# Performance work log

Measured on AMD Instinct MI355X. Metric: run time of the kernel, lower is better.

The kernel has to match this reference:

```python
import jax, jax.numpy as jnp
import numpy as np

B, S, D = 4, 2048, 1024
H = 16
HD = D // H  # 64

def setup_inputs() -> dict:
    key = jax.random.key(0)
    ks = jax.random.split(key, 7)
    s = 0.02
    return {
        "x": jax.random.normal(ks[0], (B, S, D), dtype=jnp.float32),
        "Wq": jax.random.normal(ks[1], (D, D), dtype=jnp.float32) * s,
        "bq": jax.random.normal(ks[2], (D,), dtype=jnp.float32) * s,
        "Wk": jax.random.normal(ks[3], (D, D), dtype=jnp.float32) * s,
        "bk": jax.random.normal(ks[4], (D,), dtype=jnp.float32) * s,
        "Wv": jax.random.normal(ks[5], (D, D), dtype=jnp.float32) * s,
        "bv": jax.random.normal(ks[6], (D,), dtype=jnp.float32) * s,
    }

def reference(x, Wq, bq, Wk, bk, Wv, bv):
    bs, seq, _ = x.shape
    q = (x @ Wq.T + bq).reshape(bs, seq, H, HD).transpose(0, 2, 1, 3)  # [b,h,s,d]
    k = (x @ Wk.T + bk).reshape(bs, seq, H, HD).transpose(0, 2, 1, 3)
    v = (x @ Wv.T + bv).reshape(bs, seq, H, HD).transpose(0, 2, 1, 3)
    scores = jnp.einsum('bhqd,bhkd->bhqk', q, k) / jnp.sqrt(jnp.float32(HD))
    probs = jax.nn.softmax(scores, axis=-1)  # dropout p=0 -> identity
    att = jnp.einsum('bhqk,bhkd->bhqd', probs, v)
    return att.transpose(0, 2, 1, 3).reshape(bs, seq, H * HD)
```

## Files before the change

### kernel.cpp

```cpp
#include <hip/hip_runtime.h>

typedef __bf16 bf16x8 __attribute__((ext_vector_type(8)));
typedef float f32x4 __attribute__((ext_vector_type(4)));
typedef float f32x16 __attribute__((ext_vector_type(16)));

#define BATCH 4
#define SEQ   2048
#define DIM   1024
#define NH    16
#define HD    64
#define ECF   0.18033688f

__device__ __forceinline__ unsigned short f2bf(float f) {
  union { float f; unsigned u; } v; v.f = f;
  unsigned u = v.u;
  u += 0x7FFF + ((u >> 16) & 1);
  return (unsigned short)(u >> 16);
}

__device__ __forceinline__ void g2lds16(const unsigned short* g, unsigned short* l) {
  __builtin_amdgcn_global_load_lds(
      (const __attribute__((address_space(1))) unsigned int*)g,
      (__attribute__((address_space(3))) unsigned int*)l, 16, 0, 0);
}

__device__ __forceinline__ unsigned packbf(float a, float b) {
  __bf16 lo = (__bf16)a, hi = (__bf16)b;
  unsigned short ul = __builtin_bit_cast(unsigned short, lo);
  unsigned short uh = __builtin_bit_cast(unsigned short, hi);
  return (unsigned)ul | ((unsigned)uh << 16);
}

__global__ __launch_bounds__(256) void cast_all_kernel(
    const float* __restrict__ x,  const float* __restrict__ Wq,
    const float* __restrict__ Wk, const float* __restrict__ Wv,
    unsigned short* __restrict__ xb,  unsigned short* __restrict__ wqb,
    unsigned short* __restrict__ wkb, unsigned short* __restrict__ wvb) {
  const int XG = (BATCH * SEQ * DIM) / 8;
  const int WG = (DIM * DIM) / 8;
  int i = blockIdx.x * 256 + threadIdx.x;
  const float* in; unsigned short* out; float sc = 1.0f; int off;
  if (i < XG)               { in = x;  out = xb;  off = i; }
  else if (i < XG + WG)     { in = Wq; out = wqb; off = i - XG; sc = ECF; }
  else if (i < XG + 2 * WG) { in = Wk; out = wkb; off = i - XG - WG; }
  else                      { in = Wv; out = wvb; off = i - XG - 2 * WG; }
  const float4* p = (const float4*)in + (size_t)off * 2;
  float4 a = p[0], b = p[1];
  unsigned short r[8];
  r[0] = f2bf(a.x * sc); r[1] = f2bf(a.y * sc); r[2] = f2bf(a.z * sc); r[3] = f2bf(a.w * sc);
  r[4] = f2bf(b.x * sc); r[5] = f2bf(b.y * sc); r[6] = f2bf(b.z * sc); r[7] = f2bf(b.w * sc);
  *(uint4*)&out[(size_t)off * 8] = *(uint4*)r;
}

__global__ __launch_bounds__(256) void gemm_qkv(
    const unsigned short* __restrict__ A,
    const unsigned short* __restrict__ Wqp, const unsigned short* __restrict__ Wkp,
    const unsigned short* __restrict__ Wvp,
    const float* __restrict__ bqp, const float* __restrict__ bkp,
    const float* __restrict__ bvp,
    unsigned short* __restrict__ oq, unsigned short* __restrict__ ok,
    unsigned short* __restrict__ ov) {
  __shared__ unsigned short As[128 * 32];
  __shared__ unsigned short Bs[128 * 32];
  const int z = blockIdx.z;
  const unsigned short* W = (z == 0) ? Wqp : (z == 1) ? Wkp : Wvp;
  const float* bias        = (z == 0) ? bqp : (z == 1) ? bkp : bvp;
  unsigned short* outp     = (z == 0) ? oq  : (z == 1) ? ok  : ov;
  const float bsc          = (z == 0) ? ECF : 1.0f;
  const int mode = (z == 2) ? 1 : 0;

  const int tid  = threadIdx.x;
  const int wave = tid >> 6;
  const int lane = tid & 63;
  const int lm   = lane & 15;
  const int qd   = lane >> 4;
  const int m0 = blockIdx.x * 128;
  const int n0 = blockIdx.y * 128;
  const int wm = (wave >> 1) * 64;
  const int wn = (wave & 1) * 64;

  const f32x4 zero = {0.f, 0.f, 0.f, 0.f};
  f32x4 acc[4][4];
#pragma unroll
  for (int i = 0; i < 4; ++i)
#pragma unroll
    for (int j = 0; j < 4; ++j) acc[i][j] = zero;

  const int srow = tid >> 2;
  const int scol = (((tid & 3) ^ ((tid >> 3) & 3))) * 8;
  const int cs   = (qd ^ ((lm >> 1) & 3)) * 8;

  for (int kt = 0; kt < DIM; kt += 32) {
    __syncthreads();
    g2lds16(&A[(size_t)(m0 + srow) * DIM + kt + scol],       &As[(size_t)tid * 8]);
    g2lds16(&A[(size_t)(m0 + 64 + srow) * DIM + kt + scol],  &As[2048 + (size_t)tid * 8]);
    g2lds16(&W[(size_t)(n0 + srow) * DIM + kt + scol],       &Bs[(size_t)tid * 8]);
    g2lds16(&W[(size_t)(n0 + 64 + srow) * DIM + kt + scol],  &Bs[2048 + (size_t)tid * 8]);
    __syncthreads();

    bf16x8 af[4], bfr[4];
#pragma unroll
    for (int i = 0; i < 4; ++i) af[i]  = *(const bf16x8*)&As[(wm + i * 16 + lm) * 32 + cs];
#pragma unroll
    for (int j = 0; j < 4; ++j) bfr[j] = *(const bf16x8*)&Bs[(wn + j * 16 + lm) * 32 + cs];
#pragma unroll
    for (int i = 0; i < 4; ++i)
#pragma unroll
      for (int j = 0; j < 4; ++j)
        acc[i][j] = __builtin_amdgcn_mfma_f32_16x16x32_bf16(af[i], bfr[j], acc[i][j], 0, 0, 0);
  }

#pragma unroll
  for (int j = 0; j < 4; ++j) {
    int col = n0 + wn + j * 16 + lm;
    float bb = bias[col] * bsc;
    int h = col >> 6, hd = col & 63;
#pragma unroll
    for (int i = 0; i < 4; ++i) {
      int rowb = m0 + wm + i * 16 + qd * 4;
      int b = rowb >> 11, s = rowb & 2047;
      if (mode == 0) {
#pragma unroll
        for (int r = 0; r < 4; ++r) {
          float v = acc[i][j][r] + bb;
          outp[((size_t)(b * NH + h) * SEQ + (s + r)) * HD + hd] = f2bf(v);
        }
      } else {
        unsigned short pk[4];
#pragma unroll
        for (int r = 0; r < 4; ++r) pk[r] = f2bf(acc[i][j][r] + bb);
        size_t idx = ((size_t)(b * NH + h) * HD + hd) * SEQ + s;
        *(uint2*)&outp[idx] = *(uint2*)pk;
      }
    }
  }
}

__global__ __launch_bounds__(256, 2) void flash_kernel(
    const unsigned short* __restrict__ Qp, const unsigned short* __restrict__ Kp,
    const unsigned short* __restrict__ Vp, float* __restrict__ out) {
  __shared__ __align__(16) unsigned short Ks[2][64 * 64];
  __shared__ __align__(16) unsigned short Vs[2][64 * 64];
  __shared__ float Ls[4][2][32];

  const int tid  = threadIdx.x;
  const int w    = tid >> 6;
  const int lane = tid & 63;
  const int l31  = lane & 31;
  const int hi   = lane >> 5;
  const int bh   = blockIdx.y;
  const int wq0  = blockIdx.x * 256 + w * 64;

  const unsigned short* Qb = Qp + (size_t)bh * (SEQ * HD);
  const unsigned short* Kb = Kp + (size_t)bh * (SEQ * HD);
  const unsigned short* Vb = Vp + (size_t)bh * (HD * SEQ);

  bf16x8 qf[2][4];
#pragma unroll
  for (int qb = 0; qb < 2; ++qb)
#pragma unroll
    for (int db = 0; db < 4; ++db)
      qf[qb][db] = *(const bf16x8*)&Qb[(size_t)(wq0 + qb * 32 + l31) * HD + db * 16 + hi * 8];

  f32x16 o[2][2];
#pragma unroll
  for (int qb = 0; qb < 2; ++qb)
#pragma unroll
    for (int jn = 0; jn < 2; ++jn)
#pragma unroll
      for (int r = 0; r < 16; ++r) o[qb][jn][r] = 0.f;
  float psum[2] = {0.f, 0.f};

  const int c0 = tid, c1 = tid + 256;
  const int kr0 = c0 >> 3, kp0 = ((c0 & 7) ^ (kr0 & 7)) * 8;
  const int kr1 = c1 >> 3, kp1 = ((c1 & 7) ^ (kr1 & 7)) * 8;
  const int r7 = l31 & 7;

  auto STAGE = [&](int buf, int k0) {
    g2lds16(&Kb[(size_t)(k0 + kr0) * HD + kp0], &Ks[buf][c0 * 8]);
    g2lds16(&Kb[(size_t)(k0 + kr1) * HD + kp1], &Ks[buf][c1 * 8]);
    g2lds16(&Vb[(size_t)kr0 * SEQ + k0 + kp0],  &Vs[buf][c0 * 8]);
    g2lds16(&Vb[(size_t)kr1 * SEQ + k0 + kp1],  &Vs[buf][c1 * 8]);
  };

  STAGE(0, 0);
  int cur = 0;
  for (int kt = 0; kt < SEQ / 64; ++kt) {
    __syncthreads();
    if (kt + 1 < SEQ / 64) STAGE(cur ^ 1, (kt + 1) * 64);

    const unsigned short* Kc = &Ks[cur][0];
    const unsigned short* Vc = &Vs[cur][0];

    bf16x8 pa[2][4];
#pragma unroll
    for (int kb = 0; kb < 2; ++kb) {
      f32x16 s0 = {0,0,0,0,0,0,0,0,0,0,0,0,0,0,0,0};
      f32x16 s1 = {0,0,0,0,0,0,0,0,0,0,0,0,0,0,0,0};
#pragma unroll
      for (int db = 0; db < 4; ++db) {
        int ch = (db * 2 + hi) ^ r7;
        bf16x8 kf = *(const bf16x8*)&Kc[((kb * 32 + l31) * 8 + ch) * 8];
        s0 = __builtin_amdgcn_mfma_f32_32x32x16_bf16(kf, qf[0][db], s0, 0, 0, 0);
        s1 = __builtin_amdgcn_mfma_f32_32x32x16_bf16(kf, qf[1][db], s1, 0, 0, 0);
      }
#pragma unroll
      for (int qb = 0; qb < 2; ++qb) {
        const f32x16 s = qb ? s1 : s0;
        float p[16];
#pragma unroll
        for (int r = 0; r < 16; ++r) p[r] = __builtin_amdgcn_exp2f(s[r]);
        psum[qb] += ((p[0] + p[1]) + (p[2] + p[3])) + ((p[4] + p[5]) + (p[6] + p[7]))
                  + ((p[8] + p[9]) + (p[10] + p[11])) + ((p[12] + p[13]) + (p[14] + p[15]));
        unsigned w01 = packbf(p[0],  p[1]),  w23 = packbf(p[2],  p[3]);
        unsigned w45 = packbf(p[4],  p[5]),  w67 = packbf(p[6],  p[7]);
        unsigned w89 = packbf(p[8],  p[9]),  wab = packbf(p[10], p[11]);
        unsigned wcd = packbf(p[12], p[13]), wef = packbf(p[14], p[15]);
        asm volatile("v_permlane32_swap_b32 %0, %1" : "+v"(w01), "+v"(w45));
        asm volatile("v_permlane32_swap_b32 %0, %1" : "+v"(w23), "+v"(w67));
        asm volatile("v_permlane32_swap_b32 %0, %1" : "+v"(w89), "+v"(wcd));
        asm volatile("v_permlane32_swap_b32 %0, %1" : "+v"(wab), "+v"(wef));
        union { unsigned u[4]; bf16x8 v; } flo, fhi;
        flo.u[0] = w01; flo.u[1] = w23; flo.u[2] = w45; flo.u[3] = w67;
        fhi.u[0] = w89; fhi.u[1] = wab; fhi.u[2] = wcd; fhi.u[3] = wef;
        pa[qb][kb * 2]     = flo.v;
        pa[qb][kb * 2 + 1] = fhi.v;
      }
    }

#pragma unroll
    for (int ks = 0; ks < 4; ++ks) {
#pragma unroll
      for (int jn = 0; jn < 2; ++jn) {
        int row = jn * 32 + l31;
        int ch = (ks * 2 + hi) ^ r7;
        bf16x8 vf = *(const bf16x8*)&Vc[(row * 8 + ch) * 8];
        o[0][jn] = __builtin_amdgcn_mfma_f32_32x32x16_bf16(pa[0][ks], vf, o[0][jn], 0, 0, 0);
        o[1][jn] = __builtin_amdgcn_mfma_f32_32x32x16_bf16(pa[1][ks], vf, o[1][jn], 0, 0, 0);
      }
    }
    cur ^= 1;
  }

#pragma unroll
  for (int qb = 0; qb < 2; ++qb) {
    float l = psum[qb] + __shfl_xor(psum[qb], 32);
    if (hi == 0) Ls[w][qb][l31] = 1.0f / l;
  }
  asm volatile("s_waitcnt lgkmcnt(0)" ::: "memory");

  const int b = bh >> 4, hh = bh & 15;
#pragma unroll
  for (int qb = 0; qb < 2; ++qb)
#pragma unroll
    for (int r = 0; r < 16; ++r) {
      int crow = (r & 3) + 8 * (r >> 2) + 4 * hi;
      float inv = Ls[w][qb][crow];
      int qrow = wq0 + qb * 32 + crow;
      float* po = &out[(size_t)(b * SEQ + qrow) * DIM + hh * HD + l31];
      po[0]  = o[qb][0][r] * inv;
      po[32] = o[qb][1][r] * inv;
    }
}

extern "C" void kernel_launch(void* const* d_in, const int* in_sizes, int n_in,
                              void* d_out, int out_size, void* d_ws, size_t ws_size,
                              hipStream_t stream) {
  const float* x  = (const float*)d_in[0];
  const float* Wq = (const float*)d_in[1];
  const float* bq = (const float*)d_in[2];
  const float* Wk = (const float*)d_in[3];
  const float* bk = (const float*)d_in[4];
  const float* Wv = (const float*)d_in[5];
  const float* bv = (const float*)d_in[6];
  float* out = (float*)d_out;

  unsigned short* ws = (unsigned short*)d_ws;
  const size_t XE = (size_t)BATCH * SEQ * DIM;
  const size_t WE = (size_t)DIM * DIM;
  unsigned short* xb  = ws;
  unsigned short* wqb = xb + XE;
  unsigned short* wkb = wqb + WE;
  unsigned short* wvb = wkb + WE;
  unsigned short* qb  = wvb + WE;
  unsigned short* kb  = qb + XE;
  unsigned short* vb  = kb + XE;

  const int total_groups = (int)(XE / 8 + 3 * (WE / 8));
  cast_all_kernel<<<total_groups / 256, 256, 0, stream>>>(
      x, Wq, Wk, Wv, xb, wqb, wkb, wvb);

  dim3 gg(64, 8, 3);
  gemm_qkv<<<gg, 256, 0, stream>>>(xb, wqb, wkb, wvb, bq, bk, bv, qb, kb, vb);

  dim3 fg(SEQ / 256, BATCH * NH);
  flash_kernel<<<fg, 256, 0, stream>>>(qb, kb, vb, out);
}
```

Measured before the change: 248.6 us.

## Split KV sequence across two wave groups in flash kernel with LDS combine

The flash kernel now launches 512 threads. Two groups of four waves each process half of the key sequence (first and second 1024 keys) for the same 256 query rows. The partial outputs and row sums are exchanged through shared memory and merged in the epilogue. This raises the wave count per block to hide latency, and s_setprio hints are added around the MFMA sections. The cost is double the shared-memory staging per tile, an extra LDS reduction pass, and higher register pressure under launch_bounds(512,4).

```diff
diff --git a/kernel.cpp b/kernel.cpp
--- a/kernel.cpp
+++ b/kernel.cpp
@@ -136,25 +136,31 @@
   }
 }
 
-__global__ __launch_bounds__(256, 2) void flash_kernel(
+__global__ __launch_bounds__(512, 4) void flash_kernel(
     const unsigned short* __restrict__ Qp, const unsigned short* __restrict__ Kp,
     const unsigned short* __restrict__ Vp, float* __restrict__ out) {
-  __shared__ __align__(16) unsigned short Ks[2][64 * 64];
-  __shared__ __align__(16) unsigned short Vs[2][64 * 64];
+  __shared__ __align__(16) unsigned short smem[32768];
+  __shared__ float Lpart[2][4][32];
   __shared__ float Ls[4][2][32];
 
   const int tid  = threadIdx.x;
   const int w    = tid >> 6;
+  const int sgrp = w >> 2;
+  const int qc   = w & 3;
   const int lane = tid & 63;
   const int l31  = lane & 31;
   const int hi   = lane >> 5;
   const int bh   = blockIdx.y;
-  const int wq0  = blockIdx.x * 256 + w * 64;
+  const int q0blk = blockIdx.x * 256;
+  const int wq0  = q0blk + qc * 64;
 
   const unsigned short* Qb = Qp + (size_t)bh * (SEQ * HD);
   const unsigned short* Kb = Kp + (size_t)bh * (SEQ * HD);
   const unsigned short* Vb = Vp + (size_t)bh * (HD * SEQ);
 
+  unsigned short* Ksm = smem;
+  unsigned short* Vsm = smem + 16384;
+
   bf16x8 qf[2][4];
 #pragma unroll
   for (int qb = 0; qb < 2; ++qb)
@@ -171,32 +177,28 @@
       for (int r = 0; r < 16; ++r) o[qb][jn][r] = 0.f;
   float psum[2] = {0.f, 0.f};
 
-  const int c0 = tid, c1 = tid + 256;
-  const int kr0 = c0 >> 3, kp0 = ((c0 & 7) ^ (kr0 & 7)) * 8;
-  const int kr1 = c1 >> 3, kp1 = ((c1 & 7) ^ (kr1 & 7)) * 8;
+  const int sr = tid >> 3;
+  const int sp = ((tid & 7) ^ (sr & 7)) * 8;
+
+  auto STAGE = [&](int buf, int ktile) {
+    const int kA = ktile * 64;
+    g2lds16(&Kb[(size_t)(kA + sr) * HD + sp],          &Ksm[buf * 8192 + tid * 8]);
+    g2lds16(&Kb[(size_t)(1024 + kA + sr) * HD + sp],   &Ksm[buf * 8192 + 4096 + tid * 8]);
+    g2lds16(&Vb[(size_t)sr * SEQ + kA + sp],           &Vsm[buf * 8192 + tid * 8]);
+    g2lds16(&Vb[(size_t)sr * SEQ + 1024 + kA + sp],    &Vsm[buf * 8192 + 4096 + tid * 8]);
+  };
+
   const int r7 = l31 & 7;
 
-  auto STAGE = [&](int buf, int k0) {
-    g2lds16(&Kb[(size_t)(k0 + kr0) * HD + kp0], &Ks[buf][c0 * 8]);
-    g2lds16(&Kb[(size_t)(k0 + kr1) * HD + kp1], &Ks[buf][c1 * 8]);
-    g2lds16(&Vb[(size_t)kr0 * SEQ + k0 + kp0],  &Vs[buf][c0 * 8]);
-    g2lds16(&Vb[(size_t)kr1 * SEQ + k0 + kp1],  &Vs[buf][c1 * 8]);
-  };
-
-  STAGE(0, 0);
-  int cur = 0;
-  for (int kt = 0; kt < SEQ / 64; ++kt) {
-    __syncthreads();
-    if (kt + 1 < SEQ / 64) STAGE(cur ^ 1, (kt + 1) * 64);
-
-    const unsigned short* Kc = &Ks[cur][0];
-    const unsigned short* Vc = &Vs[cur][0];
-
+  auto COMPUTE = [&](int buf) {
+    const unsigned short* Kc = &Ksm[buf * 8192 + sgrp * 4096];
+    const unsigned short* Vc = &Vsm[buf * 8192 + sgrp * 4096];
     bf16x8 pa[2][4];
 #pragma unroll
     for (int kb = 0; kb < 2; ++kb) {
       f32x16 s0 = {0,0,0,0,0,0,0,0,0,0,0,0,0,0,0,0};
       f32x16 s1 = {0,0,0,0,0,0,0,0,0,0,0,0,0,0,0,0};
+      __builtin_amdgcn_s_setprio(1);
 #pragma unroll
       for (int db = 0; db < 4; ++db) {
         int ch = (db * 2 + hi) ^ r7;
@@ -204,6 +206,7 @@
         s0 = __builtin_amdgcn_mfma_f32_32x32x16_bf16(kf, qf[0][db], s0, 0, 0, 0);
         s1 = __builtin_amdgcn_mfma_f32_32x32x16_bf16(kf, qf[1][db], s1, 0, 0, 0);
       }
+      __builtin_amdgcn_s_setprio(0);
 #pragma unroll
       for (int qb = 0; qb < 2; ++qb) {
         const f32x16 s = qb ? s1 : s0;
@@ -227,40 +230,68 @@
         pa[qb][kb * 2 + 1] = fhi.v;
       }
     }
-
+    __builtin_amdgcn_s_setprio(1);
 #pragma unroll
     for (int ks = 0; ks < 4; ++ks) {
 #pragma unroll
       for (int jn = 0; jn < 2; ++jn) {
-        int row = jn * 32 + l31;
         int ch = (ks * 2 + hi) ^ r7;
-        bf16x8 vf = *(const bf16x8*)&Vc[(row * 8 + ch) * 8];
+        bf16x8 vf = *(const bf16x8*)&Vc[((jn * 32 + l31) * 8 + ch) * 8];
         o[0][jn] = __builtin_amdgcn_mfma_f32_32x32x16_bf16(pa[0][ks], vf, o[0][jn], 0, 0, 0);
         o[1][jn] = __builtin_amdgcn_mfma_f32_32x32x16_bf16(pa[1][ks], vf, o[1][jn], 0, 0, 0);
       }
     }
-    cur ^= 1;
+    __builtin_amdgcn_s_setprio(0);
+  };
+
+  STAGE(0, 0);
+  for (int kt = 0; kt < 16; kt += 2) {
+    __syncthreads();
+    STAGE(1, kt + 1);
+    COMPUTE(0);
+    __syncthreads();
+    if (kt + 2 < 16) STAGE(0, kt + 2);
+    COMPUTE(1);
   }
 
-#pragma unroll
-  for (int qb = 0; qb < 2; ++qb) {
-    float l = psum[qb] + __shfl_xor(psum[qb], 32);
-    if (hi == 0) Ls[w][qb][l31] = 1.0f / l;
-  }
-  asm volatile("s_waitcnt lgkmcnt(0)" ::: "memory");
-
+  __syncthreads();
+  float* Op = (float*)smem;
   const int b = bh >> 4, hh = bh & 15;
-#pragma unroll
-  for (int qb = 0; qb < 2; ++qb)
-#pragma unroll
-    for (int r = 0; r < 16; ++r) {
-      int crow = (r & 3) + 8 * (r >> 2) + 4 * hi;
-      float inv = Ls[w][qb][crow];
-      int qrow = wq0 + qb * 32 + crow;
-      float* po = &out[(size_t)(b * SEQ + qrow) * DIM + hh * HD + l31];
-      po[0]  = o[qb][0][r] * inv;
-      po[32] = o[qb][1][r] * inv;
-    }
+
+#define EPI_WRITE(QB) do {                                                   \
+    _Pragma("unroll")                                                        \
+    for (int r = 0; r < 16; ++r) {                                           \
+      int crow = (r & 3) + 8 * (r >> 2) + 4 * hi;                            \
+      float* dst = &Op[(((QB) * 4 + qc) * 32 + crow) * 64 + l31];            \
+      dst[0]  = o[QB][0][r];                                                 \
+      dst[32] = o[QB][1][r];                                                 \
+    }                                                                        \
+    float lW = psum[QB] + __shfl_xor(psum[QB], 32);                          \
+    if (hi == 0) Lpart[QB][qc][l31] = lW;                                    \
+  } while (0)
+
+#define EPI_COMBINE(QB) do {                                                 \
+    float lC = psum[QB] + __shfl_xor(psum[QB], 32);                          \
+    if (hi == 0) Ls[qc][QB][l31] = 1.0f / (lC + Lpart[QB][qc][l31]);         \
+    asm volatile("s_waitcnt lgkmcnt(0)" ::: "memory");                       \
+    _Pragma("unroll")                                                        \
+    for (int r = 0; r < 16; ++r) {                                           \
+      int crow = (r & 3) + 8 * (r >> 2) + 4 * hi;                            \
+      float inv = Ls[qc][QB][crow];                                          \
+      const float* src = &Op[(((QB) * 4 + qc) * 32 + crow) * 64 + l31];      \
+      int qrow = q0blk + qc * 64 + (QB) * 32 + crow;                         \
+      float* po = &out[(size_t)(b * SEQ + qrow) * DIM + hh * HD + l31];      \
+      po[0]  = (o[QB][0][r] + src[0])  * inv;                                \
+      po[32] = (o[QB][1][r] + src[32]) * inv;                                \
+    }                                                                        \
+  } while (0)
+
+  if (sgrp == 0) EPI_WRITE(1); else EPI_WRITE(0);
+  __syncthreads();
+  if (sgrp == 0) EPI_COMBINE(0); else EPI_COMBINE(1);
+
+#undef EPI_WRITE
+#undef EPI_COMBINE
 }
 
 extern "C" void kernel_launch(void* const* d_in, const int* in_sizes, int n_in,
@@ -294,5 +325,5 @@
   gemm_qkv<<<gg, 256, 0, stream>>>(xb, wqb, wkb, wvb, bq, bk, bv, qb, kb, vb);
 
   dim3 fg(SEQ / 256, BATCH * NH);
-  flash_kernel<<<fg, 256, 0, stream>>>(qb, kb, vb, out);
-}
+  flash_kernel<<<fg, 512, 0, stream>>>(qb, kb, vb, out);
+}
```

New measurement: 702.1 us. +182.5%, slower.

## Stagger QK/PV halves across waves with setprio to overlap exp and MFMA

Applied to the files above, without the earlier changes.

Splits each 64-key tile into two 32-key halves processed in an order that alternates by wave parity, computing both QK score halves up front and then interleaving exp/pack with the PV MFMAs per half. Wave priority is raised around MFMA bursts via s_setprio so that MFMA-heavy and VALU-heavy phases of different waves overlap on the same SIMD. This adds live registers (four score accumulators at once) and relies on the hardware scheduler honoring priorities, which could raise register pressure and hurt occupancy.

```diff
diff --git a/kernel.cpp b/kernel.cpp
--- a/kernel.cpp
+++ b/kernel.cpp
@@ -145,6 +145,7 @@
 
   const int tid  = threadIdx.x;
   const int w    = tid >> 6;
+  const int wpar = w & 1;
   const int lane = tid & 63;
   const int l31  = lane & 31;
   const int hi   = lane >> 5;
@@ -192,53 +193,81 @@
     const unsigned short* Kc = &Ks[cur][0];
     const unsigned short* Vc = &Vs[cur][0];
 
-    bf16x8 pa[2][4];
-#pragma unroll
-    for (int kb = 0; kb < 2; ++kb) {
-      f32x16 s0 = {0,0,0,0,0,0,0,0,0,0,0,0,0,0,0,0};
-      f32x16 s1 = {0,0,0,0,0,0,0,0,0,0,0,0,0,0,0,0};
-#pragma unroll
-      for (int db = 0; db < 4; ++db) {
-        int ch = (db * 2 + hi) ^ r7;
-        bf16x8 kf = *(const bf16x8*)&Kc[((kb * 32 + l31) * 8 + ch) * 8];
-        s0 = __builtin_amdgcn_mfma_f32_32x32x16_bf16(kf, qf[0][db], s0, 0, 0, 0);
-        s1 = __builtin_amdgcn_mfma_f32_32x32x16_bf16(kf, qf[1][db], s1, 0, 0, 0);
-      }
-#pragma unroll
-      for (int qb = 0; qb < 2; ++qb) {
-        const f32x16 s = qb ? s1 : s0;
-        float p[16];
-#pragma unroll
-        for (int r = 0; r < 16; ++r) p[r] = __builtin_amdgcn_exp2f(s[r]);
-        psum[qb] += ((p[0] + p[1]) + (p[2] + p[3])) + ((p[4] + p[5]) + (p[6] + p[7]))
-                  + ((p[8] + p[9]) + (p[10] + p[11])) + ((p[12] + p[13]) + (p[14] + p[15]));
-        unsigned w01 = packbf(p[0],  p[1]),  w23 = packbf(p[2],  p[3]);
-        unsigned w45 = packbf(p[4],  p[5]),  w67 = packbf(p[6],  p[7]);
-        unsigned w89 = packbf(p[8],  p[9]),  wab = packbf(p[10], p[11]);
-        unsigned wcd = packbf(p[12], p[13]), wef = packbf(p[14], p[15]);
-        asm volatile("v_permlane32_swap_b32 %0, %1" : "+v"(w01), "+v"(w45));
-        asm volatile("v_permlane32_swap_b32 %0, %1" : "+v"(w23), "+v"(w67));
-        asm volatile("v_permlane32_swap_b32 %0, %1" : "+v"(w89), "+v"(wcd));
-        asm volatile("v_permlane32_swap_b32 %0, %1" : "+v"(wab), "+v"(wef));
-        union { unsigned u[4]; bf16x8 v; } flo, fhi;
-        flo.u[0] = w01; flo.u[1] = w23; flo.u[2] = w45; flo.u[3] = w67;
-        fhi.u[0] = w89; fhi.u[1] = wab; fhi.u[2] = wcd; fhi.u[3] = wef;
-        pa[qb][kb * 2]     = flo.v;
-        pa[qb][kb * 2 + 1] = fhi.v;
-      }
+    const int kbA = wpar;
+    const int kbB = wpar ^ 1;
+
+    f32x16 sA0 = {0,0,0,0,0,0,0,0,0,0,0,0,0,0,0,0};
+    f32x16 sA1 = {0,0,0,0,0,0,0,0,0,0,0,0,0,0,0,0};
+    f32x16 sB0 = {0,0,0,0,0,0,0,0,0,0,0,0,0,0,0,0};
+    f32x16 sB1 = {0,0,0,0,0,0,0,0,0,0,0,0,0,0,0,0};
+    __builtin_amdgcn_s_setprio(1);
+#pragma unroll
+    for (int db = 0; db < 4; ++db) {
+      int ch = (db * 2 + hi) ^ r7;
+      bf16x8 kf = *(const bf16x8*)&Kc[((kbA * 32 + l31) * 8 + ch) * 8];
+      sA0 = __builtin_amdgcn_mfma_f32_32x32x16_bf16(kf, qf[0][db], sA0, 0, 0, 0);
+      sA1 = __builtin_amdgcn_mfma_f32_32x32x16_bf16(kf, qf[1][db], sA1, 0, 0, 0);
     }
-
-#pragma unroll
-    for (int ks = 0; ks < 4; ++ks) {
-#pragma unroll
-      for (int jn = 0; jn < 2; ++jn) {
-        int row = jn * 32 + l31;
-        int ch = (ks * 2 + hi) ^ r7;
-        bf16x8 vf = *(const bf16x8*)&Vc[(row * 8 + ch) * 8];
-        o[0][jn] = __builtin_amdgcn_mfma_f32_32x32x16_bf16(pa[0][ks], vf, o[0][jn], 0, 0, 0);
-        o[1][jn] = __builtin_amdgcn_mfma_f32_32x32x16_bf16(pa[1][ks], vf, o[1][jn], 0, 0, 0);
-      }
+    __builtin_amdgcn_s_setprio(0);
+#pragma unroll
+    for (int db = 0; db < 4; ++db) {
+      int ch = (db * 2 + hi) ^ r7;
+      bf16x8 kf = *(const bf16x8*)&Kc[((kbB * 32 + l31) * 8 + ch) * 8];
+      sB0 = __builtin_amdgcn_mfma_f32_32x32x16_bf16(kf, qf[0][db], sB0, 0, 0, 0);
+      sB1 = __builtin_amdgcn_mfma_f32_32x32x16_bf16(kf, qf[1][db], sB1, 0, 0, 0);
     }
+
+    bf16x8 paA[2][2], paB[2][2];
+#define EXPPACK(SQ0, SQ1, PA) do {                                            \
+    _Pragma("unroll")                                                         \
+    for (int qb = 0; qb < 2; ++qb) {                                          \
+      const f32x16 s = qb ? (SQ1) : (SQ0);                                    \
+      float p[16];                                                            \
+      _Pragma("unroll")                                                       \
+      for (int r = 0; r < 16; ++r) p[r] = __builtin_amdgcn_exp2f(s[r]);       \
+      psum[qb] += ((p[0] + p[1]) + (p[2] + p[3])) + ((p[4] + p[5]) + (p[6] + p[7]))  \
+                + ((p[8] + p[9]) + (p[10] + p[11])) + ((p[12] + p[13]) + (p[14] + p[15])); \
+      unsigned w01 = packbf(p[0],  p[1]),  w23 = packbf(p[2],  p[3]);         \
+      unsigned w45 = packbf(p[4],  p[5]),  w67 = packbf(p[6],  p[7]);         \
+      unsigned w89 = packbf(p[8],  p[9]),  wab = packbf(p[10], p[11]);        \
+      unsigned wcd = packbf(p[12], p[13]), wef = packbf(p[14], p[15]);        \
+      asm volatile("v_permlane32_swap_b32 %0, %1" : "+v"(w01), "+v"(w45));    \
+      asm volatile("v_permlane32_swap_b32 %0, %1" : "+v"(w23), "+v"(w67));    \
+      asm volatile("v_permlane32_swap_b32 %0, %1" : "+v"(w89), "+v"(wcd));    \
+      asm volatile("v_permlane32_swap_b32 %0, %1" : "+v"(wab), "+v"(wef));    \
+      union { unsigned u[4]; bf16x8 v; } flo, fhi;                            \
+      flo.u[0] = w01; flo.u[1] = w23; flo.u[2] = w45; flo.u[3] = w67;         \
+      fhi.u[0] = w89; fhi.u[1] = wab; fhi.u[2] = wcd; fhi.u[3] = wef;         \
+      (PA)[qb][0] = flo.v;                                                    \
+      (PA)[qb][1] = fhi.v;                                                    \
+    }                                                                         \
+  } while (0)
+
+#define PVHALF(KB, PA) do {                                                   \
+    _Pragma("unroll")                                                         \
+    for (int ksl = 0; ksl < 2; ++ksl) {                                       \
+      int ks = (KB) * 2 + ksl;                                                \
+      _Pragma("unroll")                                                       \
+      for (int jn = 0; jn < 2; ++jn) {                                        \
+        int ch = (ks * 2 + hi) ^ r7;                                          \
+        bf16x8 vf = *(const bf16x8*)&Vc[((jn * 32 + l31) * 8 + ch) * 8];      \
+        o[0][jn] = __builtin_amdgcn_mfma_f32_32x32x16_bf16((PA)[0][ksl], vf, o[0][jn], 0, 0, 0); \
+        o[1][jn] = __builtin_amdgcn_mfma_f32_32x32x16_bf16((PA)[1][ksl], vf, o[1][jn], 0, 0, 0); \
+      }                                                                       \
+    }                                                                         \
+  } while (0)
+
+    EXPPACK(sA0, sA1, paA);
+    __builtin_amdgcn_s_setprio(1);
+    PVHALF(kbA, paA);
+    __builtin_amdgcn_s_setprio(0);
+    EXPPACK(sB0, sB1, paB);
+    __builtin_amdgcn_s_setprio(1);
+    PVHALF(kbB, paB);
+    __builtin_amdgcn_s_setprio(0);
+
+#undef EXPPACK
+#undef PVHALF
     cur ^= 1;
   }
 
```

Result: no change. 251.0 us (+1.0%).
